# Kernel optimization log

Measured on AMD Instinct MI355X. Metric: run time of the kernel, lower is better.

The kernel has to match this reference:

```python
import jax, jax.numpy as jnp
import numpy as np

NUM_VECTORS = 8192
LATENT_DIM = 256
BETA = 0.25


def setup_inputs() -> dict:
    key = jax.random.key(0)
    k1, k2 = jax.random.split(key)
    z = jax.random.normal(k1, (16, LATENT_DIM, 32, 32), dtype=jnp.float32)
    # nn.Embedding weight initialized uniform(-1/K, 1/K)
    emb_weight = jax.random.uniform(
        k2, (NUM_VECTORS, LATENT_DIM), dtype=jnp.float32,
        minval=-1.0 / NUM_VECTORS, maxval=1.0 / NUM_VECTORS)
    return {"z": z, "emb_weight": emb_weight}


def reference(z, emb_weight):
    # z: [B, C, H, W] -> [B, H, W, C]
    z_bhwc = jnp.transpose(z, (0, 2, 3, 1))
    B, H, W, C = z_bhwc.shape
    z_flat = z_bhwc.reshape(-1, C)  # [N, C]

    # Squared distances: ||z||^2 + ||e||^2 - 2 z.e  -> [N, K]
    d = (jnp.sum(z_flat ** 2, axis=1, keepdims=True)
         + jnp.sum(emb_weight ** 2, axis=1)
         - 2.0 * jnp.einsum('nc,kc->nk', z_flat, emb_weight))
    idx = jnp.argmin(d, axis=1)  # [N]

    z_q = emb_weight[idx].reshape(B, H, W, C)

    sg = jax.lax.stop_gradient
    loss = (jnp.mean((sg(z_q) - z_bhwc) ** 2)
            + BETA * jnp.mean((z_q - sg(z_bhwc)) ** 2))

    # Straight-through estimator
    z_q_st = z_bhwc + sg(z_q - z_bhwc)
    z_q_out = jnp.transpose(z_q_st, (0, 3, 1, 2))  # [B, C, H, W]
    return z_q_out, idx, loss
```

## Files before the change

kernel.cpp:

```cpp
#include <hip/hip_runtime.h>
#include <math.h>

#define NB   16
#define CC   256
#define NPTS 16384
#define KK   8192
#define Z_OUT 4194304

#define WS_ZNORM 64
#define WS_ENORM 16448
#define WS_CCNT  24640
#define WS_CIDX  41024
#define CAND_CAP 64
#define LCAP     96
#define MARGIN   4.0e-4f

typedef short v8s __attribute__((ext_vector_type(8)));
typedef float v4f __attribute__((ext_vector_type(4)));

__device__ __forceinline__ void gl_lds16(const void* g, void* l) {
    __builtin_amdgcn_global_load_lds((const __attribute__((address_space(1))) void*)g,
                                     (__attribute__((address_space(3))) void*)l, 16, 0, 0);
}
__device__ __forceinline__ unsigned short f2bf(float f) {
    unsigned int u = __float_as_uint(f);
    return (unsigned short)((u + 0x7FFFu + ((u >> 16) & 1u)) >> 16);
}
__device__ __forceinline__ unsigned fenc(float f) {
    unsigned u = __float_as_uint(f);
    return (u & 0x80000000u) ? ~u : (u | 0x80000000u);
}
__device__ __forceinline__ float fdec(unsigned m) {
    unsigned u = (m & 0x80000000u) ? (m & 0x7fffffffu) : ~m;
    return __uint_as_float(u);
}

__global__ void k_prep_z(const float* __restrict__ z, unsigned short* __restrict__ zb16) {
    __shared__ float ts[64][65];
    const int hw0 = blockIdx.x * 64, c0 = blockIdx.y * 64, b = blockIdx.z;
    const int tid = threadIdx.x;
#pragma unroll
    for (int p = 0; p < 4; ++p) {
        int u = p * 256 + tid;
        int ci = u >> 4, j4 = (u & 15) << 2;
        float4 v = *(const float4*)(z + (size_t)b * 262144 + (size_t)(c0 + ci) * 1024 + hw0 + j4);
        ts[ci][j4 + 0] = v.x; ts[ci][j4 + 1] = v.y; ts[ci][j4 + 2] = v.z; ts[ci][j4 + 3] = v.w;
    }
    __syncthreads();
#pragma unroll
    for (int p = 0; p < 4; ++p) {
        int u = p * 256 + tid;
        int hj = u >> 4, i4 = (u & 15) << 2;
        ushort4 o = make_ushort4(f2bf(ts[i4 + 0][hj]), f2bf(ts[i4 + 1][hj]),
                                 f2bf(ts[i4 + 2][hj]), f2bf(ts[i4 + 3][hj]));
        *(ushort4*)(zb16 + (size_t)(b * 1024 + hw0 + hj) * 256 + c0 + i4) = o;
    }
}

__global__ void k_tr_z(const float* __restrict__ z, float* __restrict__ zt) {
    __shared__ float ts[64][65];
    const int hw0 = blockIdx.x * 64, c0 = blockIdx.y * 64, b = blockIdx.z;
    const int tid = threadIdx.x;
#pragma unroll
    for (int p = 0; p < 4; ++p) {
        int u = p * 256 + tid;
        int ci = u >> 4, j4 = (u & 15) << 2;
        float4 v = *(const float4*)(z + (size_t)b * 262144 + (size_t)(c0 + ci) * 1024 + hw0 + j4);
        ts[ci][j4 + 0] = v.x; ts[ci][j4 + 1] = v.y; ts[ci][j4 + 2] = v.z; ts[ci][j4 + 3] = v.w;
    }
    __syncthreads();
#pragma unroll
    for (int p = 0; p < 4; ++p) {
        int u = p * 256 + tid;
        int hj = u >> 4, i4 = (u & 15) << 2;
        float4 o = make_float4(ts[i4 + 0][hj], ts[i4 + 1][hj], ts[i4 + 2][hj], ts[i4 + 3][hj]);
        *(float4*)(zt + (size_t)(b * 1024 + hw0 + hj) * 256 + c0 + i4) = o;
    }
}

__global__ void k_prep_e(const float* __restrict__ emb, unsigned short* __restrict__ ebf,
                         float* __restrict__ enorm) {
    const int w = threadIdx.x >> 6, lane = threadIdx.x & 63;
    const int k = blockIdx.x * 4 + w;
    const int i = k * CC + lane * 4;
    float4 v = *(const float4*)(emb + i);
    *(ushort4*)(ebf + i) = make_ushort4(f2bf(v.x), f2bf(v.y), f2bf(v.z), f2bf(v.w));
    float s = v.x * v.x + v.y * v.y + v.z * v.z + v.w * v.w;
    for (int off = 32; off > 0; off >>= 1) s += __shfl_down(s, off);
    if (lane == 0) enorm[k] = s;
}

__global__ void k_znorm(const float* __restrict__ z, float* __restrict__ znorm,
                        float* __restrict__ lossAcc) {
    const int n  = blockIdx.x * 256 + threadIdx.x;
    const int b  = n >> 10, hw = n & 1023;
    const float* p = z + (size_t)b * 262144 + hw;
    float s = 0.0f;
#pragma unroll 8
    for (int c = 0; c < CC; ++c) {
        float v = p[(size_t)c * 1024];
        s = fmaf(v, v, s);
    }
    znorm[n] = s;
    if (n == 0) lossAcc[0] = 0.0f;
}

__global__ __launch_bounds__(512, 2)
void k_cand(const unsigned short* __restrict__ zb16, const unsigned short* __restrict__ ebf,
            int* __restrict__ candCnt, int* __restrict__ candI) {
    __shared__ short    Bs[8][4][512];
    __shared__ unsigned runmaxU[64];
    __shared__ int      cnt[64];
    __shared__ int      lstK[64][LCAP];
    __shared__ float    lstD[64][LCAP];

    const int tid  = threadIdx.x;
    const int lane = tid & 63;
    const int w    = tid >> 6;
    const int nb   = blockIdx.x << 6;
    const int m16  = lane & 15, q = lane >> 4;

    if (tid < 64) { runmaxU[tid] = 0x007FFFFFu;  cnt[tid] = 0; }

#pragma unroll
    for (int p = 0; p < 4; ++p) {
        const int g8 = p * 8 + w;
        const int cc = g8 >> 2, nt = g8 & 3;
        const unsigned short* g = zb16 + (size_t)(nb + nt * 16 + m16) * 256 + cc * 32 + q * 8;
        gl_lds16(g, &Bs[cc][nt][lane * 8]);
    }

    auto loadA = [&](v8s (&a)[4], int kbr, int cc) {
#pragma unroll
        for (int kt = 0; kt < 4; ++kt)
            a[kt] = *(const v8s*)(ebf + (size_t)(kbr + (kt << 4) + m16) * 256 + (cc << 5) + q * 8);
    };
    auto loadB = [&](v8s (&b)[4], int cc) {
#pragma unroll
        for (int nt = 0; nt < 4; ++nt) b[nt] = *(const v8s*)&Bs[cc][nt][lane * 8];
    };

    v8s aP[4], aN[4], bP[4], bN[4];
    loadA(aP, w << 6, 0);
    __syncthreads();
    loadB(bP, 0);

#pragma unroll 1
    for (int s = 0; s < 16; ++s) {
        const int kb  = (s * 8 + w) << 6;
        const int kbn = (s < 15) ? kb + 512 : kb;
        v4f acc[16];
#pragma unroll
        for (int i = 0; i < 16; ++i) acc[i] = (v4f){0.f, 0.f, 0.f, 0.f};

#pragma unroll
        for (int cc = 0; cc < 8; ++cc) {
            if ((cc & 1) == 0) {
                loadA(aN, kb, cc + 1);
                loadB(bN, cc + 1);
#pragma unroll
                for (int kt = 0; kt < 4; ++kt)
#pragma unroll
                    for (int nt = 0; nt < 4; ++nt)
                        acc[kt * 4 + nt] = __builtin_amdgcn_mfma_f32_16x16x32_bf16(
                            aP[kt], bP[nt], acc[kt * 4 + nt], 0, 0, 0);
            } else {
                if (cc < 7) { loadA(aP, kb, cc + 1);  loadB(bP, cc + 1); }
                else        { loadA(aP, kbn, 0);      loadB(bP, 0);      }
#pragma unroll
                for (int kt = 0; kt < 4; ++kt)
#pragma unroll
                    for (int nt = 0; nt < 4; ++nt)
                        acc[kt * 4 + nt] = __builtin_amdgcn_mfma_f32_16x16x32_bf16(
                            aN[kt], bN[nt], acc[kt * 4 + nt], 0, 0, 0);
            }
        }

        float mx[4];
#pragma unroll
        for (int nt = 0; nt < 4; ++nt) {
            float m = acc[0 * 4 + nt][0];
#pragma unroll
            for (int kt = 0; kt < 4; ++kt)
#pragma unroll
                for (int r = 0; r < 4; ++r) m = fmaxf(m, acc[kt * 4 + nt][r]);
            m = fmaxf(m, __shfl_xor(m, 16));
            m = fmaxf(m, __shfl_xor(m, 32));
            mx[nt] = m;
            if (lane < 16) atomicMax(&runmaxU[nt * 16 + lane], fenc(m));
        }
#pragma unroll
        for (int nt = 0; nt < 4; ++nt) {
            const int nl = nt * 16 + m16;
            const float thr = fmaxf(fdec(runmaxU[nl]), mx[nt]) - MARGIN;
#pragma unroll
            for (int kt = 0; kt < 4; ++kt)
#pragma unroll
                for (int r = 0; r < 4; ++r) {
                    if (acc[kt * 4 + nt][r] >= thr) {
                        int k = kb + (kt << 4) + q * 4 + r;
                        int pos = atomicAdd(&cnt[nl], 1);
                        if (pos < LCAP) { lstK[nl][pos] = k; lstD[nl][pos] = acc[kt * 4 + nt][r]; }
                    }
                }
        }
        if (s == 3 || s == 9) __syncthreads();
    }

    __syncthreads();
    if (tid < 64) {
        const int n = nb + tid;
        const int c = cnt[tid];
        if (c > LCAP) {
            candCnt[n] = KK;
        } else {
            const float thr = fdec(runmaxU[tid]) - MARGIN;
            int kept = 0;
            for (int i = 0; i < c; ++i) {
                if (lstD[tid][i] >= thr) {
                    if (kept < CAND_CAP) candI[(size_t)n * CAND_CAP + kept] = lstK[tid][i];
                    ++kept;
                }
            }
            candCnt[n] = (kept > CAND_CAP) ? KK : kept;
        }
    }
}

__global__ __launch_bounds__(256)
void k_rescore2(const float* __restrict__ zt, const float* __restrict__ emb,
                const float* __restrict__ znorm, const float* __restrict__ enorm,
                const int* __restrict__ candCnt, const int* __restrict__ candI,
                float* __restrict__ idx_out) {
    const int lane = threadIdx.x & 63;
    const int n    = blockIdx.x * 4 + (threadIdx.x >> 6);
    const float zn = znorm[n];
    const int  cnt = candCnt[n];
    const float4 zv = *(const float4*)(zt + (size_t)n * CC + lane * 4);
    float bd = __builtin_inff();
    int   bk = 0x7fffffff;
    if (cnt <= CAND_CAP) {
#pragma unroll 1
        for (int i = 0; i < cnt; ++i) {
            const int k = candI[(size_t)n * CAND_CAP + i];
            const float4 ev = *(const float4*)(emb + (size_t)k * CC + lane * 4);
            float p = zv.x * ev.x;
            p = fmaf(zv.y, ev.y, p);
            p = fmaf(zv.z, ev.z, p);
            p = fmaf(zv.w, ev.w, p);
#pragma unroll
            for (int off = 1; off < 64; off <<= 1) p += __shfl_xor(p, off);
            const float d = (zn + enorm[k]) - (p + p);
            if (d < bd || (d == bd && k < bk)) { bd = d; bk = k; }
        }
    } else {
#pragma unroll 1
        for (int k = 0; k < KK; ++k) {
            const float4 ev = *(const float4*)(emb + (size_t)k * CC + lane * 4);
            float p = zv.x * ev.x;
            p = fmaf(zv.y, ev.y, p);
            p = fmaf(zv.z, ev.z, p);
            p = fmaf(zv.w, ev.w, p);
#pragma unroll
            for (int off = 1; off < 64; off <<= 1) p += __shfl_xor(p, off);
            const float d = (zn + enorm[k]) - (p + p);
            if (d < bd) { bd = d; bk = k; }
        }
    }
    if (lane == 0) idx_out[n] = (float)bk;
}

__global__ void k_gather(const float* __restrict__ z, const float* __restrict__ emb,
                         const float* __restrict__ idxf, float* __restrict__ out,
                         float* __restrict__ lossAcc) {
    __shared__ float red[256];
    const int bid = blockIdx.x;
    const int b = bid >> 5, h = bid & 31;
    const int t = threadIdx.x;
    const int w_ = t & 31, cg = t >> 5;
    const int n = b * 1024 + h * 32 + w_;
    const int ki = (int)idxf[n];
    const float* ep = emb + (size_t)ki * CC;
    const size_t base = (size_t)b * 262144 + h * 32 + w_;
    float ls = 0.0f;
#pragma unroll 4
    for (int c = cg; c < CC; c += 8) {
        float e = ep[c];
        size_t a = base + (size_t)c * 1024;
        float zv = z[a];
        out[a] = e;
        float df = e - zv;
        ls = fmaf(df, df, ls);
    }
    red[t] = ls;
    __syncthreads();
    for (int s = 128; s > 0; s >>= 1) {
        if (t < s) red[t] += red[t + s];
        __syncthreads();
    }
    if (t == 0) atomicAdd(lossAcc, red[0]);
}

__global__ void k_loss(const float* __restrict__ lossAcc, float* __restrict__ outLoss) {
    if (threadIdx.x == 0) {
        float m = lossAcc[0] * (1.0f / 4194304.0f);
        outLoss[0] = m + 0.25f * m;
    }
}

extern "C" void kernel_launch(void* const* d_in, const int* in_sizes, int n_in,
                              void* d_out, int out_size, void* d_ws, size_t ws_size,
                              hipStream_t stream) {
    const float* z   = (const float*)d_in[0];
    const float* emb = (const float*)d_in[1];
    float* outf = (float*)d_out;
    float* wsf  = (float*)d_ws;

    float* lossAcc = wsf;
    float* znorm   = wsf + WS_ZNORM;
    float* enorm   = wsf + WS_ENORM;
    int*   candCnt = (int*)(wsf + WS_CCNT);
    int*   candI   = (int*)(wsf + WS_CIDX);

    unsigned short* zb16 = (unsigned short*)outf;
    unsigned short* ebf  = (unsigned short*)(outf + 2097152);
    float* zt = outf;

    k_prep_z<<<dim3(16, 4, 16), 256, 0, stream>>>(z, zb16);
    k_prep_e<<<2048, 256, 0, stream>>>(emb, ebf, enorm);
    k_znorm<<<64, 256, 0, stream>>>(z, znorm, lossAcc);
    k_cand<<<256, 512, 0, stream>>>(zb16, ebf, candCnt, candI);
    k_tr_z<<<dim3(16, 4, 16), 256, 0, stream>>>(z, zt);
    k_rescore2<<<4096, 256, 0, stream>>>(zt, emb, znorm, enorm, candCnt, candI, outf + Z_OUT);
    k_gather<<<512, 256, 0, stream>>>(z, emb, outf + Z_OUT, outf, lossAcc);
    k_loss<<<1, 64, 0, stream>>>(lossAcc, outf + Z_OUT + NPTS);
}
```

Measured before the change: 278.4 us.

## Fuse rescoring, z-norm and gather into one kernel; keep z tile in registers

```diff
diff --git a/kernel.cpp b/kernel.cpp
--- a/kernel.cpp
+++ b/kernel.cpp
@@ -7,7 +7,6 @@
 #define KK   8192
 #define Z_OUT 4194304
 
-#define WS_ZNORM 64
 #define WS_ENORM 16448
 #define WS_CCNT  24640
 #define WS_CIDX  41024
@@ -18,10 +17,6 @@
 typedef short v8s __attribute__((ext_vector_type(8)));
 typedef float v4f __attribute__((ext_vector_type(4)));
 
-__device__ __forceinline__ void gl_lds16(const void* g, void* l) {
-    __builtin_amdgcn_global_load_lds((const __attribute__((address_space(1))) void*)g,
-                                     (__attribute__((address_space(3))) void*)l, 16, 0, 0);
-}
 __device__ __forceinline__ unsigned short f2bf(float f) {
     unsigned int u = __float_as_uint(f);
     return (unsigned short)((u + 0x7FFFu + ((u >> 16) & 1u)) >> 16);
@@ -57,29 +52,8 @@
     }
 }
 
-__global__ void k_tr_z(const float* __restrict__ z, float* __restrict__ zt) {
-    __shared__ float ts[64][65];
-    const int hw0 = blockIdx.x * 64, c0 = blockIdx.y * 64, b = blockIdx.z;
-    const int tid = threadIdx.x;
-#pragma unroll
-    for (int p = 0; p < 4; ++p) {
-        int u = p * 256 + tid;
-        int ci = u >> 4, j4 = (u & 15) << 2;
-        float4 v = *(const float4*)(z + (size_t)b * 262144 + (size_t)(c0 + ci) * 1024 + hw0 + j4);
-        ts[ci][j4 + 0] = v.x; ts[ci][j4 + 1] = v.y; ts[ci][j4 + 2] = v.z; ts[ci][j4 + 3] = v.w;
-    }
-    __syncthreads();
-#pragma unroll
-    for (int p = 0; p < 4; ++p) {
-        int u = p * 256 + tid;
-        int hj = u >> 4, i4 = (u & 15) << 2;
-        float4 o = make_float4(ts[i4 + 0][hj], ts[i4 + 1][hj], ts[i4 + 2][hj], ts[i4 + 3][hj]);
-        *(float4*)(zt + (size_t)(b * 1024 + hw0 + hj) * 256 + c0 + i4) = o;
-    }
-}
-
 __global__ void k_prep_e(const float* __restrict__ emb, unsigned short* __restrict__ ebf,
-                         float* __restrict__ enorm) {
+                         float* __restrict__ enorm, float* __restrict__ lossAcc) {
     const int w = threadIdx.x >> 6, lane = threadIdx.x & 63;
     const int k = blockIdx.x * 4 + w;
     const int i = k * CC + lane * 4;
@@ -88,27 +62,12 @@
     float s = v.x * v.x + v.y * v.y + v.z * v.z + v.w * v.w;
     for (int off = 32; off > 0; off >>= 1) s += __shfl_down(s, off);
     if (lane == 0) enorm[k] = s;
-}
-
-__global__ void k_znorm(const float* __restrict__ z, float* __restrict__ znorm,
-                        float* __restrict__ lossAcc) {
-    const int n  = blockIdx.x * 256 + threadIdx.x;
-    const int b  = n >> 10, hw = n & 1023;
-    const float* p = z + (size_t)b * 262144 + hw;
-    float s = 0.0f;
-#pragma unroll 8
-    for (int c = 0; c < CC; ++c) {
-        float v = p[(size_t)c * 1024];
-        s = fmaf(v, v, s);
-    }
-    znorm[n] = s;
-    if (n == 0) lossAcc[0] = 0.0f;
+    if (blockIdx.x == 0 && threadIdx.x == 0) lossAcc[0] = 0.0f;
 }
 
 __global__ __launch_bounds__(512, 2)
 void k_cand(const unsigned short* __restrict__ zb16, const unsigned short* __restrict__ ebf,
             int* __restrict__ candCnt, int* __restrict__ candI) {
-    __shared__ short    Bs[8][4][512];
     __shared__ unsigned runmaxU[64];
     __shared__ int      cnt[64];
     __shared__ int      lstK[64][LCAP];
@@ -119,35 +78,32 @@
     const int w    = tid >> 6;
     const int nb   = blockIdx.x << 6;
     const int m16  = lane & 15, q = lane >> 4;
+    const int nh   = w & 1;
+    const int kw   = w >> 1;
 
     if (tid < 64) { runmaxU[tid] = 0x007FFFFFu;  cnt[tid] = 0; }
 
-#pragma unroll
-    for (int p = 0; p < 4; ++p) {
-        const int g8 = p * 8 + w;
-        const int cc = g8 >> 2, nt = g8 & 3;
-        const unsigned short* g = zb16 + (size_t)(nb + nt * 16 + m16) * 256 + cc * 32 + q * 8;
-        gl_lds16(g, &Bs[cc][nt][lane * 8]);
-    }
-
-    auto loadA = [&](v8s (&a)[4], int kbr, int cc) {
-#pragma unroll
-        for (int kt = 0; kt < 4; ++kt)
+    v8s breg[2][8];
+#pragma unroll
+    for (int nt = 0; nt < 2; ++nt)
+#pragma unroll
+        for (int cc = 0; cc < 8; ++cc)
+            breg[nt][cc] = *(const v8s*)(zb16 +
+                (size_t)(nb + nh * 32 + nt * 16 + m16) * 256 + cc * 32 + q * 8);
+
+    auto loadA = [&](v8s (&a)[8], int kbr, int cc) {
+#pragma unroll
+        for (int kt = 0; kt < 8; ++kt)
             a[kt] = *(const v8s*)(ebf + (size_t)(kbr + (kt << 4) + m16) * 256 + (cc << 5) + q * 8);
     };
-    auto loadB = [&](v8s (&b)[4], int cc) {
-#pragma unroll
-        for (int nt = 0; nt < 4; ++nt) b[nt] = *(const v8s*)&Bs[cc][nt][lane * 8];
-    };
-
-    v8s aP[4], aN[4], bP[4], bN[4];
-    loadA(aP, w << 6, 0);
-    __syncthreads();
-    loadB(bP, 0);
+
+    v8s aP[8], aN[8];
+    loadA(aP, kw << 7, 0);
+    __syncthreads();
 
 #pragma unroll 1
     for (int s = 0; s < 16; ++s) {
-        const int kb  = (s * 8 + w) << 6;
+        const int kb  = ((s << 2) + kw) << 7;
         const int kbn = (s < 15) ? kb + 512 : kb;
         v4f acc[16];
 #pragma unroll
@@ -157,50 +113,49 @@
         for (int cc = 0; cc < 8; ++cc) {
             if ((cc & 1) == 0) {
                 loadA(aN, kb, cc + 1);
-                loadB(bN, cc + 1);
-#pragma unroll
-                for (int kt = 0; kt < 4; ++kt)
-#pragma unroll
-                    for (int nt = 0; nt < 4; ++nt)
-                        acc[kt * 4 + nt] = __builtin_amdgcn_mfma_f32_16x16x32_bf16(
-                            aP[kt], bP[nt], acc[kt * 4 + nt], 0, 0, 0);
+#pragma unroll
+                for (int kt = 0; kt < 8; ++kt)
+#pragma unroll
+                    for (int nt = 0; nt < 2; ++nt)
+                        acc[kt * 2 + nt] = __builtin_amdgcn_mfma_f32_16x16x32_bf16(
+                            aP[kt], breg[nt][cc], acc[kt * 2 + nt], 0, 0, 0);
             } else {
-                if (cc < 7) { loadA(aP, kb, cc + 1);  loadB(bP, cc + 1); }
-                else        { loadA(aP, kbn, 0);      loadB(bP, 0);      }
-#pragma unroll
-                for (int kt = 0; kt < 4; ++kt)
-#pragma unroll
-                    for (int nt = 0; nt < 4; ++nt)
-                        acc[kt * 4 + nt] = __builtin_amdgcn_mfma_f32_16x16x32_bf16(
-                            aN[kt], bN[nt], acc[kt * 4 + nt], 0, 0, 0);
+                if (cc < 7) loadA(aP, kb, cc + 1);
+                else        loadA(aP, kbn, 0);
+#pragma unroll
+                for (int kt = 0; kt < 8; ++kt)
+#pragma unroll
+                    for (int nt = 0; nt < 2; ++nt)
+                        acc[kt * 2 + nt] = __builtin_amdgcn_mfma_f32_16x16x32_bf16(
+                            aN[kt], breg[nt][cc], acc[kt * 2 + nt], 0, 0, 0);
             }
         }
 
-        float mx[4];
-#pragma unroll
-        for (int nt = 0; nt < 4; ++nt) {
-            float m = acc[0 * 4 + nt][0];
-#pragma unroll
-            for (int kt = 0; kt < 4; ++kt)
-#pragma unroll
-                for (int r = 0; r < 4; ++r) m = fmaxf(m, acc[kt * 4 + nt][r]);
+        float mx[2];
+#pragma unroll
+        for (int nt = 0; nt < 2; ++nt) {
+            float m = acc[nt][0];
+#pragma unroll
+            for (int kt = 0; kt < 8; ++kt)
+#pragma unroll
+                for (int r = 0; r < 4; ++r) m = fmaxf(m, acc[kt * 2 + nt][r]);
             m = fmaxf(m, __shfl_xor(m, 16));
             m = fmaxf(m, __shfl_xor(m, 32));
             mx[nt] = m;
-            if (lane < 16) atomicMax(&runmaxU[nt * 16 + lane], fenc(m));
-        }
-#pragma unroll
-        for (int nt = 0; nt < 4; ++nt) {
-            const int nl = nt * 16 + m16;
+            if (lane < 16) atomicMax(&runmaxU[nh * 32 + nt * 16 + lane], fenc(m));
+        }
+#pragma unroll
+        for (int nt = 0; nt < 2; ++nt) {
+            const int nl = nh * 32 + nt * 16 + m16;
             const float thr = fmaxf(fdec(runmaxU[nl]), mx[nt]) - MARGIN;
 #pragma unroll
-            for (int kt = 0; kt < 4; ++kt)
+            for (int kt = 0; kt < 8; ++kt)
 #pragma unroll
                 for (int r = 0; r < 4; ++r) {
-                    if (acc[kt * 4 + nt][r] >= thr) {
+                    if (acc[kt * 2 + nt][r] >= thr) {
                         int k = kb + (kt << 4) + q * 4 + r;
                         int pos = atomicAdd(&cnt[nl], 1);
-                        if (pos < LCAP) { lstK[nl][pos] = k; lstD[nl][pos] = acc[kt * 4 + nt][r]; }
+                        if (pos < LCAP) { lstK[nl][pos] = k; lstD[nl][pos] = acc[kt * 2 + nt][r]; }
                     }
                 }
         }
@@ -228,77 +183,91 @@
 }
 
 __global__ __launch_bounds__(256)
-void k_rescore2(const float* __restrict__ zt, const float* __restrict__ emb,
-                const float* __restrict__ znorm, const float* __restrict__ enorm,
-                const int* __restrict__ candCnt, const int* __restrict__ candI,
-                float* __restrict__ idx_out) {
-    const int lane = threadIdx.x & 63;
-    const int n    = blockIdx.x * 4 + (threadIdx.x >> 6);
-    const float zn = znorm[n];
-    const int  cnt = candCnt[n];
-    const float4 zv = *(const float4*)(zt + (size_t)n * CC + lane * 4);
-    float bd = __builtin_inff();
-    int   bk = 0x7fffffff;
-    if (cnt <= CAND_CAP) {
-#pragma unroll 1
-        for (int i = 0; i < cnt; ++i) {
-            const int k = candI[(size_t)n * CAND_CAP + i];
-            const float4 ev = *(const float4*)(emb + (size_t)k * CC + lane * 4);
-            float p = zv.x * ev.x;
-            p = fmaf(zv.y, ev.y, p);
-            p = fmaf(zv.z, ev.z, p);
-            p = fmaf(zv.w, ev.w, p);
-#pragma unroll
-            for (int off = 1; off < 64; off <<= 1) p += __shfl_xor(p, off);
-            const float d = (zn + enorm[k]) - (p + p);
-            if (d < bd || (d == bd && k < bk)) { bd = d; bk = k; }
-        }
-    } else {
-#pragma unroll 1
-        for (int k = 0; k < KK; ++k) {
-            const float4 ev = *(const float4*)(emb + (size_t)k * CC + lane * 4);
-            float p = zv.x * ev.x;
-            p = fmaf(zv.y, ev.y, p);
-            p = fmaf(zv.z, ev.z, p);
-            p = fmaf(zv.w, ev.w, p);
-#pragma unroll
-            for (int off = 1; off < 64; off <<= 1) p += __shfl_xor(p, off);
-            const float d = (zn + enorm[k]) - (p + p);
-            if (d < bd) { bd = d; bk = k; }
-        }
-    }
-    if (lane == 0) idx_out[n] = (float)bk;
-}
-
-__global__ void k_gather(const float* __restrict__ z, const float* __restrict__ emb,
-                         const float* __restrict__ idxf, float* __restrict__ out,
-                         float* __restrict__ lossAcc) {
+void k_final(const float* __restrict__ z, const float* __restrict__ emb,
+             const float* __restrict__ enorm, const int* __restrict__ candCnt,
+             const int* __restrict__ candI, float* __restrict__ out,
+             float* __restrict__ idxf, float* __restrict__ lossAcc) {
+    __shared__ float zl[64][260];
+    __shared__ int   kis[64];
     __shared__ float red[256];
     const int bid = blockIdx.x;
-    const int b = bid >> 5, h = bid & 31;
-    const int t = threadIdx.x;
-    const int w_ = t & 31, cg = t >> 5;
-    const int n = b * 1024 + h * 32 + w_;
-    const int ki = (int)idxf[n];
-    const float* ep = emb + (size_t)ki * CC;
-    const size_t base = (size_t)b * 262144 + h * 32 + w_;
+    const int b = bid >> 4, hw0 = (bid & 15) << 6;
+    const int tid = threadIdx.x;
+    const int lane = tid & 63, w = tid >> 6;
+
+#pragma unroll
+    for (int p = 0; p < 16; ++p) {
+        const int u = p * 256 + tid;
+        const int c = u >> 4, j4 = (u & 15) << 2;
+        float4 v = *(const float4*)(z + (size_t)b * 262144 + (size_t)c * 1024 + hw0 + j4);
+        zl[j4 + 0][c] = v.x; zl[j4 + 1][c] = v.y; zl[j4 + 2][c] = v.z; zl[j4 + 3][c] = v.w;
+    }
+    __syncthreads();
+
+#pragma unroll 1
+    for (int rr = 0; rr < 16; ++rr) {
+        const int j = w * 16 + rr;
+        const int n = b * 1024 + hw0 + j;
+        const float4 zv = *(const float4*)&zl[j][lane * 4];
+        float zn = zv.x * zv.x;
+        zn = fmaf(zv.y, zv.y, zn); zn = fmaf(zv.z, zv.z, zn); zn = fmaf(zv.w, zv.w, zn);
+#pragma unroll
+        for (int off = 1; off < 64; off <<= 1) zn += __shfl_xor(zn, off);
+        const int cnt = candCnt[n];
+        float bd = __builtin_inff();
+        int   bk = 0x7fffffff;
+        if (cnt <= CAND_CAP) {
+#pragma unroll 1
+            for (int i = 0; i < cnt; ++i) {
+                const int k = candI[(size_t)n * CAND_CAP + i];
+                const float4 ev = *(const float4*)(emb + (size_t)k * CC + lane * 4);
+                float p = zv.x * ev.x;
+                p = fmaf(zv.y, ev.y, p);
+                p = fmaf(zv.z, ev.z, p);
+                p = fmaf(zv.w, ev.w, p);
+#pragma unroll
+                for (int off = 1; off < 64; off <<= 1) p += __shfl_xor(p, off);
+                const float d = (zn + enorm[k]) - (p + p);
+                if (d < bd || (d == bd && k < bk)) { bd = d; bk = k; }
+            }
+        } else {
+#pragma unroll 1
+            for (int k = 0; k < KK; ++k) {
+                const float4 ev = *(const float4*)(emb + (size_t)k * CC + lane * 4);
+                float p = zv.x * ev.x;
+                p = fmaf(zv.y, ev.y, p);
+                p = fmaf(zv.z, ev.z, p);
+                p = fmaf(zv.w, ev.w, p);
+#pragma unroll
+                for (int off = 1; off < 64; off <<= 1) p += __shfl_xor(p, off);
+                const float d = (zn + enorm[k]) - (p + p);
+                if (d < bd) { bd = d; bk = k; }
+            }
+        }
+        if (lane == 0) { idxf[n] = (float)bk; kis[j] = bk; }
+    }
+    __syncthreads();
+
+    const int j  = lane;
+    const int cg = w;
+    const int ki0 = kis[j];
+    const float* ep = emb + (size_t)ki0 * CC;
     float ls = 0.0f;
 #pragma unroll 4
-    for (int c = cg; c < CC; c += 8) {
-        float e = ep[c];
-        size_t a = base + (size_t)c * 1024;
-        float zv = z[a];
-        out[a] = e;
+    for (int c = cg * 64; c < cg * 64 + 64; ++c) {
+        float e  = ep[c];
+        float zv = zl[j][c];
+        out[(size_t)b * 262144 + (size_t)c * 1024 + hw0 + j] = e;
         float df = e - zv;
         ls = fmaf(df, df, ls);
     }
-    red[t] = ls;
-    __syncthreads();
-    for (int s = 128; s > 0; s >>= 1) {
-        if (t < s) red[t] += red[t + s];
+    red[tid] = ls;
+    __syncthreads();
+    for (int s2 = 128; s2 > 0; s2 >>= 1) {
+        if (tid < s2) red[tid] += red[tid + s2];
         __syncthreads();
     }
-    if (t == 0) atomicAdd(lossAcc, red[0]);
+    if (tid == 0) atomicAdd(lossAcc, red[0]);
 }
 
 __global__ void k_loss(const float* __restrict__ lossAcc, float* __restrict__ outLoss) {
@@ -317,21 +286,17 @@
     float* wsf  = (float*)d_ws;
 
     float* lossAcc = wsf;
-    float* znorm   = wsf + WS_ZNORM;
     float* enorm   = wsf + WS_ENORM;
     int*   candCnt = (int*)(wsf + WS_CCNT);
     int*   candI   = (int*)(wsf + WS_CIDX);
 
     unsigned short* zb16 = (unsigned short*)outf;
     unsigned short* ebf  = (unsigned short*)(outf + 2097152);
-    float* zt = outf;
-
+
+    k_prep_e<<<2048, 256, 0, stream>>>(emb, ebf, enorm, lossAcc);
     k_prep_z<<<dim3(16, 4, 16), 256, 0, stream>>>(z, zb16);
-    k_prep_e<<<2048, 256, 0, stream>>>(emb, ebf, enorm);
-    k_znorm<<<64, 256, 0, stream>>>(z, znorm, lossAcc);
     k_cand<<<256, 512, 0, stream>>>(zb16, ebf, candCnt, candI);
-    k_tr_z<<<dim3(16, 4, 16), 256, 0, stream>>>(z, zt);
-    k_rescore2<<<4096, 256, 0, stream>>>(zt, emb, znorm, enorm, candCnt, candI, outf + Z_OUT);
-    k_gather<<<512, 256, 0, stream>>>(z, emb, outf + Z_OUT, outf, lossAcc);
+    k_final<<<256, 256, 0, stream>>>(z, emb, enorm, candCnt, candI,
+                                     outf, outf + Z_OUT, lossAcc);
     k_loss<<<1, 64, 0, stream>>>(lossAcc, outf + Z_OUT + NPTS);
 }
```

After: 398.0 us. 43.0% more time.
